# Kernel optimization log

Measured on AMD Instinct MI355X. Metric: run time of the kernel, lower is better.

The kernel has to match this reference:

```python
import jax, jax.numpy as jnp
import numpy as np

B, H, W = 4, 512, 229        # batch, time frames, mel bins (N_BINS)
C = 32                        # out_channels (model_complexity)
KT, KF = 3, 3                 # local attention window (w_size)
OUT = 88                      # output_features (MIDI pitches)


def setup_inputs() -> dict:
    key = jax.random.key(0)
    ks = jax.random.split(key, 8)
    spec = jax.random.normal(ks[0], (B, H, W), jnp.float32)
    # 1x1 conv weights [C_out, C_in]; kaiming fan_out std = sqrt(2/C_out)
    std = float(np.sqrt(2.0 / C))
    Wq = jax.random.normal(ks[1], (C, 1), jnp.float32) * std
    Wk = jax.random.normal(ks[2], (C, 1), jnp.float32) * std
    Wv = jax.random.normal(ks[3], (C, 1), jnp.float32) * std
    # relative position biases: rel_t over time offsets, rel_f over freq offsets
    rel_t = jax.random.normal(ks[4], (C // 2, KT), jnp.float32)
    rel_f = jax.random.normal(ks[5], (C // 2, KF), jnp.float32)
    W_lin = jax.random.normal(ks[6], (OUT, C * W), jnp.float32) * 0.01
    b_lin = jnp.zeros((OUT,), jnp.float32)
    return {"spec": spec, "Wq": Wq, "Wk": Wk, "Wv": Wv,
            "rel_t": rel_t, "rel_f": rel_f, "W_lin": W_lin, "b_lin": b_lin}


def _unfold(t, h, w):
    # t: [B,C,h+KT-1,w+KF-1] -> [B,C,h,w,KT,KF] (overlapping local windows)
    wins = [t[:, :, i:i + h, j:j + w] for i in range(KT) for j in range(KF)]
    s = jnp.stack(wins, axis=-1)           # [B,C,h,w,KT*KF]
    return s.reshape(t.shape[0], t.shape[1], h, w, KT, KF)


def reference(spec, Wq, Wk, Wv, rel_t, rel_f, W_lin, b_lin):
    x = spec[:, None]                       # [B,1,H,W]  (unsqueeze channel)
    pt, pf = (KT - 1) // 2, (KF - 1) // 2
    xp = jnp.pad(x, ((0, 0), (0, 0), (pt, pt), (pf, pf)))
    # 1x1 convs (no bias)
    q = jnp.einsum('oi,bihw->bohw', Wq, x)   # [B,C,H,W]
    k = jnp.einsum('oi,bihw->bohw', Wk, xp)  # [B,C,H+2pt,W+2pf]
    v = jnp.einsum('oi,bihw->bohw', Wv, xp)
    kw = _unfold(k, H, W)                    # [B,C,H,W,KT,KF]
    vw = _unfold(v, H, W)
    half = C // 2
    # add relative position biases to split halves of key channels
    k_t = kw[:, :half] + rel_t[None, :, None, None, :, None]
    k_f = kw[:, half:] + rel_f[None, :, None, None, None, :]
    kw = jnp.concatenate([k_t, k_f], axis=1).reshape(B, C, H, W, KT * KF)
    vw = vw.reshape(B, C, H, W, KT * KF)
    # energy: dot product over channels per spatial location -> [B,H,W,K]
    energy = jnp.einsum('bchw,bchwk->bhwk', q, kw)
    attn = jax.nn.softmax(energy, axis=-1)
    out = jnp.einsum('bhwk,bchwk->bchw', attn, vw)   # [B,C,H,W]
    # transpose(1,2).flatten(2): [B,H,C,W] -> [B,H,C*W]
    feat = jnp.transpose(out, (0, 2, 1, 3)).reshape(B, H, C * W)
    frame_pred = jax.nn.sigmoid(feat @ W_lin.T + b_lin)   # [B,H,OUT]
    attn_out = attn[:, None]                # [B,groups=1,H,W,K]
    return frame_pred, attn_out
```

## Files before the change

### kernel.cpp

```cpp
#include <hip/hip_runtime.h>
#include <math.h>

#define Bn 4
#define Hn 512
#define Wn 229
#define Cn 32
#define OUTn 88
#define BH (Bn*Hn)
#define NPOS (BH*Wn)
#define FP_SIZE (BH*OUTn)
#define CW (Cn*Wn)

#define WS_SCAL 0
#define WS_WEFF 16
#define WS_O    (16 + Wn*OUTn)

__global__ __launch_bounds__(256) void prep_kernel(
    const float* __restrict__ Wq, const float* __restrict__ Wk,
    const float* __restrict__ Wv, const float* __restrict__ rel_t,
    const float* __restrict__ rel_f, const float* __restrict__ W_lin,
    float* __restrict__ ws) {
  int tid = blockIdx.x * 256 + threadIdx.x;
  if (tid == 0) {
    float A = 0.f;
    for (int c = 0; c < Cn; ++c) A += Wq[c] * Wk[c];
    ws[WS_SCAL + 0] = A;
    for (int i = 0; i < 3; ++i) {
      float rt = 0.f, rf = 0.f;
      for (int c = 0; c < 16; ++c) {
        rt += Wq[c]      * rel_t[c*3 + i];
        rf += Wq[16 + c] * rel_f[c*3 + i];
      }
      ws[WS_SCAL + 1 + i] = rt;
      ws[WS_SCAL + 4 + i] = rf;
    }
  }
  if (tid < Wn * OUTn) {
    int w = tid / OUTn;
    int o = tid - w * OUTn;
    float acc = 0.f;
    #pragma unroll
    for (int c = 0; c < Cn; ++c) acc += W_lin[o*CW + c*Wn + w] * Wv[c];
    ws[WS_WEFF + tid] = acc;
  }
}

__global__ __launch_bounds__(256) void attn_kernel(
    const float* __restrict__ spec, const float* __restrict__ ws,
    float* __restrict__ out, float* __restrict__ o_ws) {
  __shared__ float satt[256 * 9];
  const int idx = blockIdx.x * 256 + threadIdx.x;
  const int bh  = idx / Wn;
  const int w   = idx - bh * Wn;
  const int h   = bh & (Hn - 1);

  const float A  = ws[WS_SCAL + 0];
  const float s  = spec[idx];

  float e[9], sp[9];
  float m = -1e30f;
  #pragma unroll
  for (int i = 0; i < 3; ++i) {
    const int hh = h + i - 1;
    const bool hin = (unsigned)hh < (unsigned)Hn;
    const float rt = ws[WS_SCAL + 1 + i];
    #pragma unroll
    for (int j = 0; j < 3; ++j) {
      const int ww = w + j - 1;
      const bool in = hin && ((unsigned)ww < (unsigned)Wn);
      const int k = i*3 + j;
      const float v = in ? spec[idx + (i-1)*Wn + (j-1)] : 0.f;
      sp[k] = v;
      const float ek = s * (A*v + rt + ws[WS_SCAL + 4 + j]);
      e[k] = ek;
      m = fmaxf(m, ek);
    }
  }
  float sum = 0.f;
  #pragma unroll
  for (int k = 0; k < 9; ++k) { e[k] = __expf(e[k] - m); sum += e[k]; }
  const float inv = 1.f / sum;
  float o = 0.f;
  #pragma unroll
  for (int k = 0; k < 9; ++k) {
    const float a = e[k] * inv;
    satt[threadIdx.x * 9 + k] = a;
    o += a * sp[k];
  }
  o_ws[w * BH + bh] = o;

  __syncthreads();
  float* dst = out + FP_SIZE + (size_t)blockIdx.x * (256 * 9);
  #pragma unroll
  for (int k = 0; k < 9; ++k)
    dst[k * 256 + threadIdx.x] = satt[k * 256 + threadIdx.x];
}

__global__ __launch_bounds__(256) void head_kernel(
    const float* __restrict__ ws, const float* __restrict__ b_lin,
    float* __restrict__ out) {
  const int og = blockIdx.x % 11;
  const int bh = (blockIdx.x / 11) * 256 + threadIdx.x;
  const float* WeffT = ws + WS_WEFF;
  const float* ovec  = ws + WS_O;

  float acc[8];
  #pragma unroll
  for (int u = 0; u < 8; ++u) acc[u] = b_lin[og*8 + u];

  for (int w = 0; w < Wn; ++w) {
    const float x = ovec[w * BH + bh];
    const float* wr = WeffT + w * OUTn + og * 8;
    #pragma unroll
    for (int u = 0; u < 8; ++u) acc[u] += wr[u] * x;
  }
  float* d = out + bh * OUTn + og * 8;
  #pragma unroll
  for (int u = 0; u < 8; ++u) d[u] = 1.f / (1.f + __expf(-acc[u]));
}

extern "C" void kernel_launch(void* const* d_in, const int* in_sizes, int n_in,
                              void* d_out, int out_size, void* d_ws, size_t ws_size,
                              hipStream_t stream) {
  const float* spec  = (const float*)d_in[0];
  const float* Wq    = (const float*)d_in[1];
  const float* Wk    = (const float*)d_in[2];
  const float* Wv    = (const float*)d_in[3];
  const float* rel_t = (const float*)d_in[4];
  const float* rel_f = (const float*)d_in[5];
  const float* W_lin = (const float*)d_in[6];
  const float* b_lin = (const float*)d_in[7];
  float* out = (float*)d_out;
  float* ws  = (float*)d_ws;

  prep_kernel<<<(Wn*OUTn + 255)/256, 256, 0, stream>>>(Wq, Wk, Wv, rel_t, rel_f, W_lin, ws);
  attn_kernel<<<NPOS/256, 256, 0, stream>>>(spec, ws, out, ws + WS_O);
  head_kernel<<<88, 256, 0, stream>>>(ws, b_lin, out);
}
```

Baseline: 111.7 us.

## Compute attention scalars per block, coalesce prep reads, halve head block size

Each attention block now computes the seven scalar dot products (q·k and q·rel biases) itself in shared memory instead of reading them from a prep kernel. This removes the attention kernel's dependency on prep and the single serial thread that used to compute the scalars. Prep now reads W_lin coalesced along w and stages Wv in shared memory. The attention-map store uses float4. The head kernel uses 128-thread blocks, doubling the block count, with an unrolled w loop and vectorised output stores. The cost is redundant scalar work in every attention block and an extra barrier.

Result: slower. 122.3 us (+9.5%).

```diff
diff --git a/kernel.cpp b/kernel.cpp
--- a/kernel.cpp
+++ b/kernel.cpp
@@ -11,51 +11,60 @@
 #define FP_SIZE (BH*OUTn)
 #define CW (Cn*Wn)
 
-#define WS_SCAL 0
 #define WS_WEFF 16
 #define WS_O    (16 + Wn*OUTn)
 
 __global__ __launch_bounds__(256) void prep_kernel(
-    const float* __restrict__ Wq, const float* __restrict__ Wk,
-    const float* __restrict__ Wv, const float* __restrict__ rel_t,
-    const float* __restrict__ rel_f, const float* __restrict__ W_lin,
+    const float* __restrict__ Wv, const float* __restrict__ W_lin,
     float* __restrict__ ws) {
-  int tid = blockIdx.x * 256 + threadIdx.x;
-  if (tid == 0) {
-    float A = 0.f;
-    for (int c = 0; c < Cn; ++c) A += Wq[c] * Wk[c];
-    ws[WS_SCAL + 0] = A;
-    for (int i = 0; i < 3; ++i) {
-      float rt = 0.f, rf = 0.f;
-      for (int c = 0; c < 16; ++c) {
-        rt += Wq[c]      * rel_t[c*3 + i];
-        rf += Wq[16 + c] * rel_f[c*3 + i];
-      }
-      ws[WS_SCAL + 1 + i] = rt;
-      ws[WS_SCAL + 4 + i] = rf;
-    }
-  }
-  if (tid < Wn * OUTn) {
-    int w = tid / OUTn;
-    int o = tid - w * OUTn;
-    float acc = 0.f;
-    #pragma unroll
-    for (int c = 0; c < Cn; ++c) acc += W_lin[o*CW + c*Wn + w] * Wv[c];
-    ws[WS_WEFF + tid] = acc;
-  }
+  __shared__ float wv[Cn];
+  if (threadIdx.x < Cn) wv[threadIdx.x] = Wv[threadIdx.x];
+  __syncthreads();
+  const int tid = blockIdx.x * 256 + threadIdx.x;
+  if (tid >= Wn * OUTn) return;
+  const int o = tid / Wn;
+  const int w = tid - o * Wn;
+  const float* src = W_lin + o * CW + w;
+  float acc = 0.f;
+  #pragma unroll
+  for (int c = 0; c < Cn; ++c) acc += src[c * Wn] * wv[c];
+  ws[WS_WEFF + w * OUTn + o] = acc;
 }
 
 __global__ __launch_bounds__(256) void attn_kernel(
-    const float* __restrict__ spec, const float* __restrict__ ws,
+    const float* __restrict__ spec,
+    const float* __restrict__ Wq, const float* __restrict__ Wk,
+    const float* __restrict__ rel_t, const float* __restrict__ rel_f,
     float* __restrict__ out, float* __restrict__ o_ws) {
-  __shared__ float satt[256 * 9];
+  __shared__ float scal[8];
+  __shared__ __align__(16) float satt[256 * 9];
+
+  if (threadIdx.x < 7) {
+    const int t = threadIdx.x;
+    float acc = 0.f;
+    if (t == 0) {
+      #pragma unroll
+      for (int c = 0; c < Cn; ++c) acc += Wq[c] * Wk[c];
+    } else if (t < 4) {
+      const int i = t - 1;
+      #pragma unroll
+      for (int c = 0; c < 16; ++c) acc += Wq[c] * rel_t[c*3 + i];
+    } else {
+      const int j = t - 4;
+      #pragma unroll
+      for (int c = 0; c < 16; ++c) acc += Wq[16 + c] * rel_f[c*3 + j];
+    }
+    scal[t] = acc;
+  }
+  __syncthreads();
+
   const int idx = blockIdx.x * 256 + threadIdx.x;
   const int bh  = idx / Wn;
   const int w   = idx - bh * Wn;
   const int h   = bh & (Hn - 1);
 
-  const float A  = ws[WS_SCAL + 0];
-  const float s  = spec[idx];
+  const float A = scal[0];
+  const float s = spec[idx];
 
   float e[9], sp[9];
   float m = -1e30f;
@@ -63,7 +72,7 @@
   for (int i = 0; i < 3; ++i) {
     const int hh = h + i - 1;
     const bool hin = (unsigned)hh < (unsigned)Hn;
-    const float rt = ws[WS_SCAL + 1 + i];
+    const float rt = scal[1 + i];
     #pragma unroll
     for (int j = 0; j < 3; ++j) {
       const int ww = w + j - 1;
@@ -71,7 +80,7 @@
       const int k = i*3 + j;
       const float v = in ? spec[idx + (i-1)*Wn + (j-1)] : 0.f;
       sp[k] = v;
-      const float ek = s * (A*v + rt + ws[WS_SCAL + 4 + j]);
+      const float ek = s * (fmaf(A, v, rt) + scal[4 + j]);
       e[k] = ek;
       m = fmaxf(m, ek);
     }
@@ -85,22 +94,29 @@
   for (int k = 0; k < 9; ++k) {
     const float a = e[k] * inv;
     satt[threadIdx.x * 9 + k] = a;
-    o += a * sp[k];
+    o = fmaf(a, sp[k], o);
   }
   o_ws[w * BH + bh] = o;
 
   __syncthreads();
-  float* dst = out + FP_SIZE + (size_t)blockIdx.x * (256 * 9);
+  float4* dst4 = (float4*)(out + FP_SIZE + (size_t)blockIdx.x * 2304);
+  const float4* s4 = (const float4*)satt;
   #pragma unroll
-  for (int k = 0; k < 9; ++k)
-    dst[k * 256 + threadIdx.x] = satt[k * 256 + threadIdx.x];
+  for (int r = 0; r < 2; ++r) {
+    const int p = r * 256 + threadIdx.x;
+    dst4[p] = s4[p];
+  }
+  {
+    const int p = 512 + threadIdx.x;
+    if (p < 576) dst4[p] = s4[p];
+  }
 }
 
-__global__ __launch_bounds__(256) void head_kernel(
+__global__ __launch_bounds__(128) void head_kernel(
     const float* __restrict__ ws, const float* __restrict__ b_lin,
     float* __restrict__ out) {
   const int og = blockIdx.x % 11;
-  const int bh = (blockIdx.x / 11) * 256 + threadIdx.x;
+  const int bh = (blockIdx.x / 11) * 128 + threadIdx.x;
   const float* WeffT = ws + WS_WEFF;
   const float* ovec  = ws + WS_O;
 
@@ -108,15 +124,21 @@
   #pragma unroll
   for (int u = 0; u < 8; ++u) acc[u] = b_lin[og*8 + u];
 
+  #pragma unroll 4
   for (int w = 0; w < Wn; ++w) {
     const float x = ovec[w * BH + bh];
     const float* wr = WeffT + w * OUTn + og * 8;
     #pragma unroll
-    for (int u = 0; u < 8; ++u) acc[u] += wr[u] * x;
+    for (int u = 0; u < 8; ++u) acc[u] = fmaf(wr[u], x, acc[u]);
   }
-  float* d = out + bh * OUTn + og * 8;
-  #pragma unroll
-  for (int u = 0; u < 8; ++u) d[u] = 1.f / (1.f + __expf(-acc[u]));
+
+  float4 r0, r1;
+  r0.x = 1.f/(1.f+__expf(-acc[0])); r0.y = 1.f/(1.f+__expf(-acc[1]));
+  r0.z = 1.f/(1.f+__expf(-acc[2])); r0.w = 1.f/(1.f+__expf(-acc[3]));
+  r1.x = 1.f/(1.f+__expf(-acc[4])); r1.y = 1.f/(1.f+__expf(-acc[5]));
+  r1.z = 1.f/(1.f+__expf(-acc[6])); r1.w = 1.f/(1.f+__expf(-acc[7]));
+  float4* d = (float4*)(out + (size_t)bh * OUTn + og * 8);
+  d[0] = r0; d[1] = r1;
 }
 
 extern "C" void kernel_launch(void* const* d_in, const int* in_sizes, int n_in,
@@ -133,7 +155,7 @@
   float* out = (float*)d_out;
   float* ws  = (float*)d_ws;
 
-  prep_kernel<<<(Wn*OUTn + 255)/256, 256, 0, stream>>>(Wq, Wk, Wv, rel_t, rel_f, W_lin, ws);
-  attn_kernel<<<NPOS/256, 256, 0, stream>>>(spec, ws, out, ws + WS_O);
-  head_kernel<<<88, 256, 0, stream>>>(ws, b_lin, out);
+  attn_kernel<<<NPOS/256, 256, 0, stream>>>(spec, Wq, Wk, rel_t, rel_f, out, ws + WS_O);
+  prep_kernel<<<(Wn*OUTn + 255)/256, 256, 0, stream>>>(Wv, W_lin, ws);
+  head_kernel<<<176, 128, 0, stream>>>(ws, b_lin, out);
 }
```
